# Kernel optimization log

Hardware: AMD Instinct MI355X
Metric: run time of the kernel (lower is better)

Reference implementation:

```python
import jax, jax.numpy as jnp
import numpy as np

NUM_NODES = 2048
NUM_REL = 8
HIDDEN = 256


def setup_inputs() -> dict:
    key = jax.random.key(0)
    k1, k2, k3 = jax.random.split(key, 3)
    X = jax.random.normal(k1, (NUM_NODES, HIDDEN, NUM_REL), dtype=jnp.float32)
    A = jax.random.uniform(k2, (NUM_NODES, NUM_NODES, NUM_REL), dtype=jnp.float32)
    # nn.init.normal_(std=0.01)
    weight = 0.01 * jax.random.normal(k3, (HIDDEN, HIDDEN, NUM_REL), dtype=jnp.float32)
    return {"X": X, "A": A, "weight": weight}


def _tensor_product(A, B):
    # Faithful to the original: FFT along last (relation) dim, take REAL part of
    # both transformed operands, per-slice matmul, then real part of ifft.
    Af = jnp.real(jnp.fft.fft(A, axis=-1))  # (n1, n2, k)
    Bf = jnp.real(jnp.fft.fft(B, axis=-1))  # (n2, n4, k)
    C = jnp.einsum('nmk,mhk->nhk', Af, Bf)  # batched real matmul over slices k
    return jnp.real(jnp.fft.ifft(C, axis=-1)).astype(A.dtype)


def reference(X, A, weight):
    res = _tensor_product(A, X)          # (num_nodes, hidden, num_rel)
    res = _tensor_product(res, weight)   # (num_nodes, hidden, num_rel)
    return res
```

## Files before the change

### kernel.cpp

```cpp
#include <hip/hip_runtime.h>


typedef __bf16 bf16_t;
typedef __bf16 bf16x2 __attribute__((ext_vector_type(2)));
typedef __bf16 bf16x8 __attribute__((ext_vector_type(8)));
typedef float f32x4 __attribute__((ext_vector_type(4)));

#define R2C 0.70710678118654752f

__device__ __forceinline__ size_t swz(int r, int c, int K) {
  return (size_t)r * K + (c & ~63) + ((((c >> 3) & 7) ^ (r & 7)) << 3) + (c & 7);
}

__device__ __forceinline__ void async_cp16(const void* g, void* l) {
  __builtin_amdgcn_global_load_lds((const __attribute__((address_space(1))) char*)g,
                                   (__attribute__((address_space(3))) char*)l,
                                   16, 0, 0);
}

__device__ __forceinline__ void fwd5(const float x[8], float F[5]) {
  float s04 = x[0] + x[4], d04 = x[0] - x[4];
  float s26 = x[2] + x[6];
  float s15 = x[1] + x[5], s37 = x[3] + x[7];
  float t = (x[1] + x[7]) - (x[3] + x[5]);
  float e = s04 + s26, o = s15 + s37;
  F[0] = e + o;
  F[1] = d04 + R2C * t;
  F[2] = s04 - s26;
  F[3] = d04 - R2C * t;
  F[4] = e - o;
}

__global__ __launch_bounds__(256) void k_pre(const float* __restrict__ X,
                                             const float* __restrict__ A,
                                             const float* __restrict__ W,
                                             bf16_t* __restrict__ Xft,
                                             bf16_t* __restrict__ Af,
                                             bf16_t* __restrict__ Wft) {
  __shared__ bf16_t tx[40][256];
  int b = blockIdx.x;
  if (b < 2048) {
    size_t t = (size_t)b * 256 + threadIdx.x;
    size_t idx = t * 8;
    int n = (int)(idx >> 11), m0 = (int)(idx & 2047);
    const float4* p = (const float4*)(A + idx * 8);
    float F[8][5];
#pragma unroll
    for (int u = 0; u < 8; u++) {
      float4 a = p[2 * u], bq = p[2 * u + 1];
      float x[8] = {a.x, a.y, a.z, a.w, bq.x, bq.y, bq.z, bq.w};
      fwd5(x, F[u]);
    }
    size_t pos = (size_t)n * 2048 + (m0 & ~63) +
                 ((((m0 >> 3) & 7) ^ (n & 7)) << 3);
#pragma unroll
    for (int j = 0; j < 5; j++) {
      bf16x8 v;
#pragma unroll
      for (int u = 0; u < 8; u++) v[u] = (bf16_t)F[u][j];
      *(bf16x8*)(Af + (size_t)j * 4194304 + pos) = v;
    }
  } else if (b < 2304) {
    int bx = b - 2048;
    int m0 = (bx & 7) * 256, h0 = (bx >> 3) * 8;
    int t = threadIdx.x;
    const float4* p = (const float4*)(X + (((size_t)(m0 + t) * 256) + h0) * 8);
#pragma unroll
    for (int h = 0; h < 8; h++) {
      float4 a = p[2 * h], bb = p[2 * h + 1];
      float x[8] = {a.x, a.y, a.z, a.w, bb.x, bb.y, bb.z, bb.w};
      float F[5];
      fwd5(x, F);
#pragma unroll
      for (int j = 0; j < 5; j++) tx[j * 8 + h][t] = (bf16_t)F[j];
    }
    __syncthreads();
#pragma unroll
    for (int it = 0; it < 5; it++) {
      int slot = it * 256 + t;
      int row = slot >> 5, ch = slot & 31;
      int j = row >> 3, hl = row & 7;
      int h = h0 + hl;
      size_t gpos = (size_t)j * 524288 + (size_t)h * 2048 + m0 +
                    ((ch & ~7) << 3) + (((ch & 7) ^ (h & 7)) << 3);
      *(uint4*)(Xft + gpos) = *(const uint4*)(&tx[row][ch * 8]);
    }
  } else {
    int h = b - 2304;
    int hp = threadIdx.x;
    const float4* p = (const float4*)(W + ((size_t)hp * 256 + h) * 8);
    float4 a = p[0], bb = p[1];
    float x[8] = {a.x, a.y, a.z, a.w, bb.x, bb.y, bb.z, bb.w};
    float F[5];
    fwd5(x, F);
    const float sc[5] = {0.125f, 0.25f, 0.25f, 0.25f, 0.125f};
    size_t pos = swz(h, hp, 256);
#pragma unroll
    for (int j = 0; j < 5; j++)
      Wft[(size_t)j * 65536 + pos] = (bf16_t)(F[j] * sc[j]);
  }
}

__global__ __launch_bounds__(256) void gemm_ring(const bf16_t* __restrict__ A,
                                                 const bf16_t* __restrict__ B,
                                                 bf16_t* __restrict__ C, int K,
                                                 size_t ap, size_t bp, size_t cp) {
  __shared__ bf16_t sm[65536];
  const int j = blockIdx.z;
  const bf16_t* Aj = A + (size_t)j * ap;
  const bf16_t* Bj = B + (size_t)j * bp;
  bf16_t* Cj = C + (size_t)j * cp;
  const int n0 = blockIdx.x * 128, h0 = blockIdx.y * 128;
  const int tid = threadIdx.x;
  const int wv = tid >> 6, ln = tid & 63;
  const int quad = ln >> 4, l16 = ln & 15;
  const int wn = (wv & 1) * 64, wh = (wv >> 1) * 64;

  const bf16_t* ga[4];
  const bf16_t* gb[4];
  int lo[4];
#pragma unroll
  for (int s = 0; s < 4; s++) {
    int slot = s * 256 + tid;
    int row = slot >> 3, c16 = slot & 7;
    ga[s] = Aj + (size_t)(n0 + row) * K + c16 * 8;
    gb[s] = Bj + (size_t)(h0 + row) * K + c16 * 8;
    lo[s] = (s * 256 + wv * 64) * 8;
  }

  const int T = K >> 6;
#pragma unroll
  for (int i = 0; i < 3; i++) {
#pragma unroll
    for (int s = 0; s < 4; s++) {
      async_cp16(ga[s] + i * 64, sm + i * 8192 + lo[s]);
      async_cp16(gb[s] + i * 64, sm + 32768 + i * 8192 + lo[s]);
    }
  }

  f32x4 acc[4][4] = {};
  for (int t = 0; t < T; t++) {
    int b = t & 3;
    if (t + 3 < T) {
      int nb = (t + 3) & 3;
#pragma unroll
      for (int s = 0; s < 4; s++) {
        async_cp16(ga[s] + (t + 3) * 64, sm + nb * 8192 + lo[s]);
        async_cp16(gb[s] + (t + 3) * 64, sm + 32768 + nb * 8192 + lo[s]);
      }
      __builtin_amdgcn_s_waitcnt(0x4F78);
    } else if (t + 2 < T) {
      __builtin_amdgcn_s_waitcnt(0x4F70);
    } else if (t + 1 < T) {
      __builtin_amdgcn_s_waitcnt(0xF78);
    } else {
      __builtin_amdgcn_s_waitcnt(0xF70);
    }
    __builtin_amdgcn_s_barrier();
    const bf16_t* Asp = sm + b * 8192;
    const bf16_t* Bsp = sm + 32768 + b * 8192;
#pragma unroll
    for (int kh = 0; kh < 2; kh++) {
      bf16x8 af[4], bfr[4];
      int c16 = kh * 4 + quad;
#pragma unroll
      for (int i = 0; i < 4; i++) {
        int ra = wn + i * 16 + l16;
        int rb = wh + i * 16 + l16;
        af[i] = *(const bf16x8*)(Asp + ra * 64 + ((c16 ^ (ra & 7)) << 3));
        bfr[i] = *(const bf16x8*)(Bsp + rb * 64 + ((c16 ^ (rb & 7)) << 3));
      }
#pragma unroll
      for (int i = 0; i < 4; i++)
#pragma unroll
        for (int t2 = 0; t2 < 4; t2++)
          acc[i][t2] = __builtin_amdgcn_mfma_f32_16x16x32_bf16(af[i], bfr[t2],
                                                               acc[i][t2], 0, 0, 0);
    }
    __builtin_amdgcn_s_barrier();
  }
#pragma unroll
  for (int i = 0; i < 4; i++) {
#pragma unroll
    for (int t = 0; t < 4; t++) {
      int hc = h0 + wh + t * 16 + l16;
#pragma unroll
      for (int rg = 0; rg < 4; rg++) {
        int nr = n0 + wn + i * 16 + quad * 4 + rg;
        Cj[swz(nr, hc, 256)] = (bf16_t)acc[i][t][rg];
      }
    }
  }
}

__global__ __launch_bounds__(256) void gemm_fc(const bf16_t* __restrict__ C1,
                                               const bf16_t* __restrict__ Wf,
                                               float* __restrict__ out) {
  __shared__ bf16_t sm[65536];
  const int n0 = blockIdx.x * 64, h0 = blockIdx.y * 64;
  const int tid = threadIdx.x;
  const int wv = tid >> 6, ln = tid & 63;
  const int quad = ln >> 4, l16 = ln & 15;
  const int wn = (wv & 1) * 32, wh = (wv >> 1) * 32;

  const int srow = (tid >> 5), sc8 = (tid & 31) * 8;
  const int lbase = wv * 512;

#define STAGE_J(jj)                                                          \
  {                                                                          \
    const bf16_t* Aj = C1 + (size_t)(jj)*524288 + (size_t)n0 * 256;          \
    const bf16_t* Bj = Wf + (size_t)(jj)*65536 + (size_t)h0 * 256;           \
    bf16_t* da = sm + ((jj)&1) * 32768;                                      \
    bf16_t* db = da + 16384;                                                 \
    _Pragma("unroll") for (int s = 0; s < 8; s++) {                          \
      async_cp16(Aj + (size_t)(s * 8 + srow) * 256 + sc8, da + s * 2048 + lbase); \
      async_cp16(Bj + (size_t)(s * 8 + srow) * 256 + sc8, db + s * 2048 + lbase); \
    }                                                                        \
  }

  const float CKJ[5][5] = {
      {1.f, 1.f, 1.f, 1.f, 1.f},
      {1.f, R2C, 0.f, -R2C, -1.f},
      {1.f, 0.f, -1.f, 0.f, 1.f},
      {1.f, -R2C, 0.f, R2C, -1.f},
      {1.f, -1.f, 1.f, -1.f, 1.f}};

  f32x4 outk[5][2][2] = {};

  STAGE_J(0);
#pragma unroll
  for (int j = 0; j < 5; j++) {
    if (j < 4) {
      STAGE_J(j + 1);
      __builtin_amdgcn_s_waitcnt(0x4F70);
    } else {
      __builtin_amdgcn_s_waitcnt(0xF70);
    }
    __builtin_amdgcn_s_barrier();
    const bf16_t* Ab = sm + (j & 1) * 32768;
    const bf16_t* Bb = Ab + 16384;
    f32x4 acc[2][2] = {};
#pragma unroll
    for (int kh = 0; kh < 8; kh++) {
      int c16 = kh * 4 + quad;
      int cb = (c16 & ~7) << 3;
      bf16x8 af[2], bfr[2];
#pragma unroll
      for (int i = 0; i < 2; i++) {
        int ra = wn + i * 16 + l16;
        int rb = wh + i * 16 + l16;
        af[i] = *(const bf16x8*)(Ab + ra * 256 + cb + (((c16 & 7) ^ (ra & 7)) << 3));
        bfr[i] = *(const bf16x8*)(Bb + rb * 256 + cb + (((c16 & 7) ^ (rb & 7)) << 3));
      }
#pragma unroll
      for (int i = 0; i < 2; i++)
#pragma unroll
        for (int t = 0; t < 2; t++)
          acc[i][t] = __builtin_amdgcn_mfma_f32_16x16x32_bf16(af[i], bfr[t],
                                                              acc[i][t], 0, 0, 0);
    }
#pragma unroll
    for (int k = 0; k < 5; k++) {
      if (CKJ[j][k] != 0.f) {
#pragma unroll
        for (int i = 0; i < 2; i++)
#pragma unroll
          for (int t = 0; t < 2; t++)
#pragma unroll
            for (int rg = 0; rg < 4; rg++)
              outk[k][i][t][rg] += CKJ[j][k] * acc[i][t][rg];
      }
    }
    __builtin_amdgcn_s_barrier();
  }

#pragma unroll
  for (int i = 0; i < 2; i++) {
#pragma unroll
    for (int rg = 0; rg < 4; rg++) {
      int n = n0 + wn + i * 16 + quad * 4 + rg;
#pragma unroll
      for (int t = 0; t < 2; t++) {
        int h = h0 + wh + t * 16 + l16;
        float c0 = outk[0][i][t][rg], c1 = outk[1][i][t][rg];
        float c2 = outk[2][i][t][rg], c3 = outk[3][i][t][rg];
        float c4 = outk[4][i][t][rg];
        float4* op = (float4*)(out + (size_t)n * 2048 + h * 8);
        op[0] = make_float4(c0, c1, c2, c3);
        op[1] = make_float4(c4, c3, c2, c1);
      }
    }
  }
#undef STAGE_J
}

extern "C" void kernel_launch(void* const* d_in, const int* in_sizes, int n_in,
                              void* d_out, int out_size, void* d_ws, size_t ws_size,
                              hipStream_t stream) {
  const float* X = (const float*)d_in[0];
  const float* A = (const float*)d_in[1];
  const float* W = (const float*)d_in[2];
  float* out = (float*)d_out;
  char* ws = (char*)d_ws;

  bf16_t* Af  = (bf16_t*)(ws);
  bf16_t* Xft = (bf16_t*)(ws + 41943040);
  bf16_t* Wft = (bf16_t*)(ws + 47185920);
  bf16_t* C1  = (bf16_t*)(ws + 47841280);

  k_pre<<<dim3(2560), 256, 0, stream>>>(X, A, W, Xft, Af, Wft);
  gemm_ring<<<dim3(16, 2, 5), 256, 0, stream>>>(
      Af, Xft, C1, 2048, (size_t)4194304, (size_t)524288, (size_t)524288);
  gemm_fc<<<dim3(32, 4), 256, 0, stream>>>(C1, Wft, out);
}
```

Before: 253.8 us.

## Fuse FFT preprocessing and ring GEMM into one persistent kernel with flag sync

Merges the FFT/bf16 conversion kernel and the batched ring GEMM into a single launch of 320 blocks. 160 producer blocks transform W, X and A in K-chunks and bump per-chunk atomic counters, while 160 GEMM blocks spin-wait on those counters before streaming each chunk. The aim is to overlap the memory-bound A transform with MFMA work and drop a kernel boundary. In exchange the GEMM pipeline shrinks from a 4-stage to a 2-stage LDS ring and adds spin-waits. It also relies on producers and consumers being co-resident, which risks deadlock.

After: 337.7 us. 33.1% more time.

```diff
diff --git a/kernel.cpp b/kernel.cpp
--- a/kernel.cpp
+++ b/kernel.cpp
@@ -2,7 +2,6 @@
 
 
 typedef __bf16 bf16_t;
-typedef __bf16 bf16x2 __attribute__((ext_vector_type(2)));
 typedef __bf16 bf16x8 __attribute__((ext_vector_type(8)));
 typedef float f32x4 __attribute__((ext_vector_type(4)));
 
@@ -31,163 +30,176 @@
   F[4] = e - o;
 }
 
-__global__ __launch_bounds__(256) void k_pre(const float* __restrict__ X,
-                                             const float* __restrict__ A,
-                                             const float* __restrict__ W,
-                                             bf16_t* __restrict__ Xft,
-                                             bf16_t* __restrict__ Af,
-                                             bf16_t* __restrict__ Wft) {
-  __shared__ bf16_t tx[40][256];
-  int b = blockIdx.x;
-  if (b < 2048) {
-    size_t t = (size_t)b * 256 + threadIdx.x;
-    size_t idx = t * 8;
-    int n = (int)(idx >> 11), m0 = (int)(idx & 2047);
-    const float4* p = (const float4*)(A + idx * 8);
-    float F[8][5];
-#pragma unroll
-    for (int u = 0; u < 8; u++) {
-      float4 a = p[2 * u], bq = p[2 * u + 1];
-      float x[8] = {a.x, a.y, a.z, a.w, bq.x, bq.y, bq.z, bq.w};
-      fwd5(x, F[u]);
-    }
-    size_t pos = (size_t)n * 2048 + (m0 & ~63) +
-                 ((((m0 >> 3) & 7) ^ (n & 7)) << 3);
-#pragma unroll
-    for (int j = 0; j < 5; j++) {
-      bf16x8 v;
-#pragma unroll
-      for (int u = 0; u < 8; u++) v[u] = (bf16_t)F[u][j];
-      *(bf16x8*)(Af + (size_t)j * 4194304 + pos) = v;
-    }
-  } else if (b < 2304) {
-    int bx = b - 2048;
-    int m0 = (bx & 7) * 256, h0 = (bx >> 3) * 8;
-    int t = threadIdx.x;
-    const float4* p = (const float4*)(X + (((size_t)(m0 + t) * 256) + h0) * 8);
-#pragma unroll
-    for (int h = 0; h < 8; h++) {
-      float4 a = p[2 * h], bb = p[2 * h + 1];
+__global__ __launch_bounds__(256, 2) void k_fused(
+    const float* __restrict__ X, const float* __restrict__ A,
+    const float* __restrict__ W, bf16_t* __restrict__ Xft,
+    bf16_t* __restrict__ Af, bf16_t* __restrict__ Wft,
+    bf16_t* __restrict__ C1, int* __restrict__ flags) {
+  __shared__ bf16_t sm[32768];
+  const int tid = threadIdx.x;
+  const int b = blockIdx.x;
+
+  if (b >= 160) {
+    const int pid = b - 160;
+
+    for (int h = pid; h < 256; h += 160) {
+      const float4* p = (const float4*)(W + ((size_t)tid * 256 + h) * 8);
+      float4 a = p[0], bb = p[1];
       float x[8] = {a.x, a.y, a.z, a.w, bb.x, bb.y, bb.z, bb.w};
       float F[5];
       fwd5(x, F);
-#pragma unroll
-      for (int j = 0; j < 5; j++) tx[j * 8 + h][t] = (bf16_t)F[j];
+      const float sc[5] = {0.125f, 0.25f, 0.25f, 0.25f, 0.125f};
+      size_t pos = swz(h, tid, 256);
+#pragma unroll
+      for (int j = 0; j < 5; j++)
+        Wft[(size_t)j * 65536 + pos] = (bf16_t)(F[j] * sc[j]);
+    }
+
+    bf16_t(*tx)[256] = (bf16_t(*)[256])sm;
+    for (int v = pid; v < 512; v += 160) {
+      int c = v >> 6, i = v & 63;
+      if (i < 32) {
+        int m0 = c * 256, h0 = i * 8;
+        const float4* p = (const float4*)(X + (((size_t)(m0 + tid) * 256) + h0) * 8);
+#pragma unroll
+        for (int h = 0; h < 8; h++) {
+          float4 a = p[2 * h], bb = p[2 * h + 1];
+          float x[8] = {a.x, a.y, a.z, a.w, bb.x, bb.y, bb.z, bb.w};
+          float F[5];
+          fwd5(x, F);
+#pragma unroll
+          for (int j = 0; j < 5; j++) tx[j * 8 + h][tid] = (bf16_t)F[j];
+        }
+        __syncthreads();
+#pragma unroll
+        for (int it = 0; it < 5; it++) {
+          int slot = it * 256 + tid;
+          int row = slot >> 5, ch = slot & 31;
+          int j = row >> 3, hl = row & 7;
+          int h = h0 + hl;
+          size_t gpos = (size_t)j * 524288 + (size_t)h * 2048 + m0 +
+                        ((ch & ~7) << 3) + (((ch & 7) ^ (h & 7)) << 3);
+          *(uint4*)(Xft + gpos) = *(const uint4*)(&tx[row][ch * 8]);
+        }
+      } else {
+        int n0 = (i - 32) * 64, mb = c * 256;
+#pragma unroll
+        for (int w = 0; w < 8; w++) {
+          int tw = w * 256 + tid;
+          int n = n0 + (tw >> 5), m0u = mb + (tw & 31) * 8;
+          const float4* p = (const float4*)(A + ((size_t)n * 2048 + m0u) * 8);
+          float F[8][5];
+#pragma unroll
+          for (int u = 0; u < 8; u++) {
+            float4 a = p[2 * u], bq = p[2 * u + 1];
+            float x[8] = {a.x, a.y, a.z, a.w, bq.x, bq.y, bq.z, bq.w};
+            fwd5(x, F[u]);
+          }
+          size_t pos = (size_t)n * 2048 + (m0u & ~63) +
+                       ((((m0u >> 3) & 7) ^ (n & 7)) << 3);
+#pragma unroll
+          for (int j = 0; j < 5; j++) {
+            bf16x8 vv;
+#pragma unroll
+            for (int u = 0; u < 8; u++) vv[u] = (bf16_t)F[u][j];
+            *(bf16x8*)(Af + (size_t)j * 4194304 + pos) = vv;
+          }
+        }
+      }
+      __syncthreads();
+      if (tid == 0) {
+        __threadfence();
+        atomicAdd(&flags[c], 1);
+      }
+    }
+  } else {
+    const int j = b >> 5, y = (b >> 4) & 1, x = b & 15;
+    const bf16_t* Aj = Af + (size_t)j * 4194304;
+    const bf16_t* Bj = Xft + (size_t)j * 524288;
+    bf16_t* Cj = C1 + (size_t)j * 524288;
+    const int n0 = x * 128, h0 = y * 128;
+    const int wv = tid >> 6, ln = tid & 63;
+    const int quad = ln >> 4, l16 = ln & 15;
+    const int wn = (wv & 1) * 64, wh = (wv >> 1) * 64;
+
+    const bf16_t* ga[4];
+    const bf16_t* gb[4];
+    int lo[4];
+#pragma unroll
+    for (int s = 0; s < 4; s++) {
+      int slot = s * 256 + tid;
+      int row = slot >> 3, c16 = slot & 7;
+      ga[s] = Aj + (size_t)(n0 + row) * 2048 + c16 * 8;
+      gb[s] = Bj + (size_t)(h0 + row) * 2048 + c16 * 8;
+      lo[s] = (s * 256 + wv * 64) * 8;
+    }
+
+    if (tid == 0) {
+      while (atomicAdd(&flags[0], 0) < 64) __builtin_amdgcn_s_sleep(8);
+      __threadfence();
     }
     __syncthreads();
 #pragma unroll
-    for (int it = 0; it < 5; it++) {
-      int slot = it * 256 + t;
-      int row = slot >> 5, ch = slot & 31;
-      int j = row >> 3, hl = row & 7;
-      int h = h0 + hl;
-      size_t gpos = (size_t)j * 524288 + (size_t)h * 2048 + m0 +
-                    ((ch & ~7) << 3) + (((ch & 7) ^ (h & 7)) << 3);
-      *(uint4*)(Xft + gpos) = *(const uint4*)(&tx[row][ch * 8]);
-    }
-  } else {
-    int h = b - 2304;
-    int hp = threadIdx.x;
-    const float4* p = (const float4*)(W + ((size_t)hp * 256 + h) * 8);
-    float4 a = p[0], bb = p[1];
-    float x[8] = {a.x, a.y, a.z, a.w, bb.x, bb.y, bb.z, bb.w};
-    float F[5];
-    fwd5(x, F);
-    const float sc[5] = {0.125f, 0.25f, 0.25f, 0.25f, 0.125f};
-    size_t pos = swz(h, hp, 256);
-#pragma unroll
-    for (int j = 0; j < 5; j++)
-      Wft[(size_t)j * 65536 + pos] = (bf16_t)(F[j] * sc[j]);
-  }
-}
-
-__global__ __launch_bounds__(256) void gemm_ring(const bf16_t* __restrict__ A,
-                                                 const bf16_t* __restrict__ B,
-                                                 bf16_t* __restrict__ C, int K,
-                                                 size_t ap, size_t bp, size_t cp) {
-  __shared__ bf16_t sm[65536];
-  const int j = blockIdx.z;
-  const bf16_t* Aj = A + (size_t)j * ap;
-  const bf16_t* Bj = B + (size_t)j * bp;
-  bf16_t* Cj = C + (size_t)j * cp;
-  const int n0 = blockIdx.x * 128, h0 = blockIdx.y * 128;
-  const int tid = threadIdx.x;
-  const int wv = tid >> 6, ln = tid & 63;
-  const int quad = ln >> 4, l16 = ln & 15;
-  const int wn = (wv & 1) * 64, wh = (wv >> 1) * 64;
-
-  const bf16_t* ga[4];
-  const bf16_t* gb[4];
-  int lo[4];
-#pragma unroll
-  for (int s = 0; s < 4; s++) {
-    int slot = s * 256 + tid;
-    int row = slot >> 3, c16 = slot & 7;
-    ga[s] = Aj + (size_t)(n0 + row) * K + c16 * 8;
-    gb[s] = Bj + (size_t)(h0 + row) * K + c16 * 8;
-    lo[s] = (s * 256 + wv * 64) * 8;
-  }
-
-  const int T = K >> 6;
-#pragma unroll
-  for (int i = 0; i < 3; i++) {
-#pragma unroll
     for (int s = 0; s < 4; s++) {
-      async_cp16(ga[s] + i * 64, sm + i * 8192 + lo[s]);
-      async_cp16(gb[s] + i * 64, sm + 32768 + i * 8192 + lo[s]);
-    }
-  }
-
-  f32x4 acc[4][4] = {};
-  for (int t = 0; t < T; t++) {
-    int b = t & 3;
-    if (t + 3 < T) {
-      int nb = (t + 3) & 3;
-#pragma unroll
-      for (int s = 0; s < 4; s++) {
-        async_cp16(ga[s] + (t + 3) * 64, sm + nb * 8192 + lo[s]);
-        async_cp16(gb[s] + (t + 3) * 64, sm + 32768 + nb * 8192 + lo[s]);
-      }
-      __builtin_amdgcn_s_waitcnt(0x4F78);
-    } else if (t + 2 < T) {
-      __builtin_amdgcn_s_waitcnt(0x4F70);
-    } else if (t + 1 < T) {
-      __builtin_amdgcn_s_waitcnt(0xF78);
-    } else {
-      __builtin_amdgcn_s_waitcnt(0xF70);
-    }
-    __builtin_amdgcn_s_barrier();
-    const bf16_t* Asp = sm + b * 8192;
-    const bf16_t* Bsp = sm + 32768 + b * 8192;
-#pragma unroll
-    for (int kh = 0; kh < 2; kh++) {
-      bf16x8 af[4], bfr[4];
-      int c16 = kh * 4 + quad;
-#pragma unroll
-      for (int i = 0; i < 4; i++) {
-        int ra = wn + i * 16 + l16;
-        int rb = wh + i * 16 + l16;
-        af[i] = *(const bf16x8*)(Asp + ra * 64 + ((c16 ^ (ra & 7)) << 3));
-        bfr[i] = *(const bf16x8*)(Bsp + rb * 64 + ((c16 ^ (rb & 7)) << 3));
-      }
-#pragma unroll
-      for (int i = 0; i < 4; i++)
-#pragma unroll
-        for (int t2 = 0; t2 < 4; t2++)
-          acc[i][t2] = __builtin_amdgcn_mfma_f32_16x16x32_bf16(af[i], bfr[t2],
-                                                               acc[i][t2], 0, 0, 0);
-    }
-    __builtin_amdgcn_s_barrier();
-  }
-#pragma unroll
-  for (int i = 0; i < 4; i++) {
-#pragma unroll
-    for (int t = 0; t < 4; t++) {
-      int hc = h0 + wh + t * 16 + l16;
-#pragma unroll
-      for (int rg = 0; rg < 4; rg++) {
-        int nr = n0 + wn + i * 16 + quad * 4 + rg;
-        Cj[swz(nr, hc, 256)] = (bf16_t)acc[i][t][rg];
+      async_cp16(ga[s], sm + lo[s]);
+      async_cp16(gb[s], sm + 16384 + lo[s]);
+    }
+
+    f32x4 acc[4][4] = {};
+    for (int t = 0; t < 32; t++) {
+      int p = t & 1;
+      if (t < 31) {
+        if (((t + 1) & 3) == 0) {
+          if (tid == 0) {
+            while (atomicAdd(&flags[(t + 1) >> 2], 0) < 64)
+              __builtin_amdgcn_s_sleep(8);
+            __threadfence();
+          }
+          __syncthreads();
+        }
+        int np = p ^ 1;
+#pragma unroll
+        for (int s = 0; s < 4; s++) {
+          async_cp16(ga[s] + (t + 1) * 64, sm + np * 8192 + lo[s]);
+          async_cp16(gb[s] + (t + 1) * 64, sm + 16384 + np * 8192 + lo[s]);
+        }
+        __builtin_amdgcn_s_waitcnt(0xF78);
+      } else {
+        __builtin_amdgcn_s_waitcnt(0xF70);
+      }
+      __builtin_amdgcn_s_barrier();
+      const bf16_t* Asp = sm + p * 8192;
+      const bf16_t* Bsp = sm + 16384 + p * 8192;
+#pragma unroll
+      for (int kh = 0; kh < 2; kh++) {
+        bf16x8 af[4], bfr[4];
+        int c16 = kh * 4 + quad;
+#pragma unroll
+        for (int i = 0; i < 4; i++) {
+          int ra = wn + i * 16 + l16;
+          int rb = wh + i * 16 + l16;
+          af[i] = *(const bf16x8*)(Asp + ra * 64 + ((c16 ^ (ra & 7)) << 3));
+          bfr[i] = *(const bf16x8*)(Bsp + rb * 64 + ((c16 ^ (rb & 7)) << 3));
+        }
+#pragma unroll
+        for (int i = 0; i < 4; i++)
+#pragma unroll
+          for (int t2 = 0; t2 < 4; t2++)
+            acc[i][t2] = __builtin_amdgcn_mfma_f32_16x16x32_bf16(
+                af[i], bfr[t2], acc[i][t2], 0, 0, 0);
+      }
+      __builtin_amdgcn_s_barrier();
+    }
+#pragma unroll
+    for (int i = 0; i < 4; i++) {
+#pragma unroll
+      for (int t = 0; t < 4; t++) {
+        int hc = h0 + wh + t * 16 + l16;
+#pragma unroll
+        for (int rg = 0; rg < 4; rg++) {
+          int nr = n0 + wn + i * 16 + quad * 4 + rg;
+          Cj[swz(nr, hc, 256)] = (bf16_t)acc[i][t][rg];
+        }
       }
     }
   }
@@ -307,9 +319,9 @@
   bf16_t* Xft = (bf16_t*)(ws + 41943040);
   bf16_t* Wft = (bf16_t*)(ws + 47185920);
   bf16_t* C1  = (bf16_t*)(ws + 47841280);
-
-  k_pre<<<dim3(2560), 256, 0, stream>>>(X, A, W, Xft, Af, Wft);
-  gemm_ring<<<dim3(16, 2, 5), 256, 0, stream>>>(
-      Af, Xft, C1, 2048, (size_t)4194304, (size_t)524288, (size_t)524288);
+  int* flags  = (int*)   (ws + 53084160);
+
+  hipMemsetAsync(flags, 0, 64, stream);
+  k_fused<<<dim3(320), 256, 0, stream>>>(X, A, W, Xft, Af, Wft, C1, flags);
   gemm_fc<<<dim3(32, 4), 256, 0, stream>>>(C1, Wft, out);
 }
```

## Halve gemm_ring M-tile and switch to double-buffered smaller LDS pipeline

Applied to the files above, without the earlier changes.

The first batched GEMM now uses 64x128 tiles instead of 128x128, which doubles the grid from 160 to 320 blocks so the MI355X's many CUs are better filled. The 4-stage async LDS ring becomes a 2-stage double buffer, shrinking shared memory from 128KB to 48KB so more blocks can reside per CU. The trade-off is less operand reuse per block, more global traffic for the B operand, and less prefetch depth to hide latency.

Measured after the change: 251.8 us. No clear change (-0.8%).

```diff
diff --git a/kernel.cpp b/kernel.cpp
--- a/kernel.cpp
+++ b/kernel.cpp
@@ -2,7 +2,6 @@
 
 
 typedef __bf16 bf16_t;
-typedef __bf16 bf16x2 __attribute__((ext_vector_type(2)));
 typedef __bf16 bf16x8 __attribute__((ext_vector_type(8)));
 typedef float f32x4 __attribute__((ext_vector_type(4)));
 
@@ -105,73 +104,75 @@
                                                  const bf16_t* __restrict__ B,
                                                  bf16_t* __restrict__ C, int K,
                                                  size_t ap, size_t bp, size_t cp) {
-  __shared__ bf16_t sm[65536];
+  __shared__ bf16_t sm[24576];
   const int j = blockIdx.z;
   const bf16_t* Aj = A + (size_t)j * ap;
   const bf16_t* Bj = B + (size_t)j * bp;
   bf16_t* Cj = C + (size_t)j * cp;
-  const int n0 = blockIdx.x * 128, h0 = blockIdx.y * 128;
+  const int n0 = blockIdx.x * 64, h0 = blockIdx.y * 128;
   const int tid = threadIdx.x;
   const int wv = tid >> 6, ln = tid & 63;
   const int quad = ln >> 4, l16 = ln & 15;
-  const int wn = (wv & 1) * 64, wh = (wv >> 1) * 64;
-
-  const bf16_t* ga[4];
+  const int wn = (wv & 1) * 32, wh = (wv >> 1) * 64;
+
+  const bf16_t* ga[2];
   const bf16_t* gb[4];
-  int lo[4];
+  int loa[2], lob[4];
+#pragma unroll
+  for (int s = 0; s < 2; s++) {
+    int slot = s * 256 + tid;
+    int row = slot >> 3, c16 = slot & 7;
+    ga[s] = Aj + (size_t)(n0 + row) * K + c16 * 8;
+    loa[s] = (s * 256 + wv * 64) * 8;
+  }
 #pragma unroll
   for (int s = 0; s < 4; s++) {
     int slot = s * 256 + tid;
     int row = slot >> 3, c16 = slot & 7;
-    ga[s] = Aj + (size_t)(n0 + row) * K + c16 * 8;
     gb[s] = Bj + (size_t)(h0 + row) * K + c16 * 8;
-    lo[s] = (s * 256 + wv * 64) * 8;
+    lob[s] = (s * 256 + wv * 64) * 8;
   }
 
   const int T = K >> 6;
 #pragma unroll
-  for (int i = 0; i < 3; i++) {
-#pragma unroll
-    for (int s = 0; s < 4; s++) {
-      async_cp16(ga[s] + i * 64, sm + i * 8192 + lo[s]);
-      async_cp16(gb[s] + i * 64, sm + 32768 + i * 8192 + lo[s]);
-    }
-  }
-
-  f32x4 acc[4][4] = {};
+  for (int s = 0; s < 2; s++) async_cp16(ga[s], sm + loa[s]);
+#pragma unroll
+  for (int s = 0; s < 4; s++) async_cp16(gb[s], sm + 8192 + lob[s]);
+
+  f32x4 acc[2][4] = {};
   for (int t = 0; t < T; t++) {
-    int b = t & 3;
-    if (t + 3 < T) {
-      int nb = (t + 3) & 3;
-#pragma unroll
-      for (int s = 0; s < 4; s++) {
-        async_cp16(ga[s] + (t + 3) * 64, sm + nb * 8192 + lo[s]);
-        async_cp16(gb[s] + (t + 3) * 64, sm + 32768 + nb * 8192 + lo[s]);
-      }
-      __builtin_amdgcn_s_waitcnt(0x4F78);
-    } else if (t + 2 < T) {
-      __builtin_amdgcn_s_waitcnt(0x4F70);
-    } else if (t + 1 < T) {
-      __builtin_amdgcn_s_waitcnt(0xF78);
+    int p = t & 1;
+    if (t + 1 < T) {
+      int np = p ^ 1;
+#pragma unroll
+      for (int s = 0; s < 2; s++)
+        async_cp16(ga[s] + (t + 1) * 64, sm + np * 4096 + loa[s]);
+#pragma unroll
+      for (int s = 0; s < 4; s++)
+        async_cp16(gb[s] + (t + 1) * 64, sm + 8192 + np * 8192 + lob[s]);
+      __builtin_amdgcn_s_waitcnt(0xF76);
     } else {
       __builtin_amdgcn_s_waitcnt(0xF70);
     }
     __builtin_amdgcn_s_barrier();
-    const bf16_t* Asp = sm + b * 8192;
-    const bf16_t* Bsp = sm + 32768 + b * 8192;
+    const bf16_t* Asp = sm + p * 4096;
+    const bf16_t* Bsp = sm + 8192 + p * 8192;
 #pragma unroll
     for (int kh = 0; kh < 2; kh++) {
-      bf16x8 af[4], bfr[4];
+      bf16x8 af[2], bfr[4];
       int c16 = kh * 4 + quad;
 #pragma unroll
+      for (int i = 0; i < 2; i++) {
+        int ra = wn + i * 16 + l16;
+        af[i] = *(const bf16x8*)(Asp + ra * 64 + ((c16 ^ (ra & 7)) << 3));
+      }
+#pragma unroll
       for (int i = 0; i < 4; i++) {
-        int ra = wn + i * 16 + l16;
         int rb = wh + i * 16 + l16;
-        af[i] = *(const bf16x8*)(Asp + ra * 64 + ((c16 ^ (ra & 7)) << 3));
         bfr[i] = *(const bf16x8*)(Bsp + rb * 64 + ((c16 ^ (rb & 7)) << 3));
       }
 #pragma unroll
-      for (int i = 0; i < 4; i++)
+      for (int i = 0; i < 2; i++)
 #pragma unroll
         for (int t2 = 0; t2 < 4; t2++)
           acc[i][t2] = __builtin_amdgcn_mfma_f32_16x16x32_bf16(af[i], bfr[t2],
@@ -180,7 +181,7 @@
     __builtin_amdgcn_s_barrier();
   }
 #pragma unroll
-  for (int i = 0; i < 4; i++) {
+  for (int i = 0; i < 2; i++) {
 #pragma unroll
     for (int t = 0; t < 4; t++) {
       int hc = h0 + wh + t * 16 + l16;
@@ -309,7 +310,7 @@
   bf16_t* C1  = (bf16_t*)(ws + 47841280);
 
   k_pre<<<dim3(2560), 256, 0, stream>>>(X, A, W, Xft, Af, Wft);
-  gemm_ring<<<dim3(16, 2, 5), 256, 0, stream>>>(
+  gemm_ring<<<dim3(32, 2, 5), 256, 0, stream>>>(
       Af, Xft, C1, 2048, (size_t)4194304, (size_t)524288, (size_t)524288);
   gemm_fc<<<dim3(32, 4), 256, 0, stream>>>(C1, Wft, out);
 }
```
